# Optimization experiments

Measured on AMD Instinct MI355X. Metric: run time of the kernel, lower is better.

The kernel has to match this reference:

```python
import jax, jax.numpy as jnp
import numpy as np

N_SERIES = 1024  # N; x carries 3N stacked time-synchronous nodes
GCN_DEPTH = 2
IN_DIM = 64
H_DIM = 64


def setup_inputs() -> dict:
    key = jax.random.key(0)
    k = jax.random.split(key, 6)
    B, C, N3 = 64, IN_DIM, 3 * N_SERIES
    x = jax.random.normal(k[0], (N3, B, C), dtype=jnp.float32)
    A = jax.random.normal(k[1], (N3, N3), dtype=jnp.float32) * 0.02
    # Linear2d (1x1 conv) params per depth; act='glu' -> out = 2*h_dim
    s0 = 1.0 / np.sqrt(IN_DIM)
    s1 = 1.0 / np.sqrt(H_DIM)
    W0 = jax.random.uniform(k[2], (2 * H_DIM, IN_DIM), jnp.float32, -s0, s0)
    b0 = jax.random.uniform(k[3], (2 * H_DIM,), jnp.float32, -s0, s0)
    W1 = jax.random.uniform(k[4], (2 * H_DIM, H_DIM), jnp.float32, -s1, s1)
    b1 = jax.random.uniform(k[5], (2 * H_DIM,), jnp.float32, -s1, s1)
    return {"x": x, "A": A, "W0": W0, "b0": b0, "W1": W1, "b1": b1}


def reference(x, A, W0, b0, W1, b1):
    # x: (3N, B, C) -> (B, C, 3N)
    h = jnp.transpose(x, (1, 2, 0))
    convs = []
    for W, b in ((W0, b0), (W1, b1)):
        # GCN2d flow='tgt_to_src': h[b,c,v] = sum_w h[b,c,w] * A[v,w]  (L=1 squeezed)
        g = jnp.einsum('bcw,vw->bcv', h, A)
        # Linear2d 1x1 conv: channels C -> 2*h_dim, then GLU gate
        y = jnp.einsum('oc,bcv->bov', W, g) + b[None, :, None]
        lhs, rhs = jnp.split(y, 2, axis=1)
        h = lhs * jax.nn.sigmoid(rhs)          # (B, h_dim, 3N)
        convs.append(jnp.transpose(h, (2, 0, 1)))  # (3N, B, h_dim)
    # crop the middle N nodes of each depth, then max over depth
    cropped = jnp.stack([c[N_SERIES:2 * N_SERIES] for c in convs], axis=0)
    return jnp.max(cropped, axis=0)  # (N, B, h_dim)
```

## Files before the change

kernel.cpp:

```cpp
#include <hip/hip_runtime.h>
#include <hip/hip_bf16.h>
#include <stdint.h>

typedef __attribute__((ext_vector_type(8))) short s16x8;
typedef __attribute__((ext_vector_type(4))) float f32x4;
typedef __attribute__((ext_vector_type(8))) unsigned short u16x8;
typedef __attribute__((ext_vector_type(4))) unsigned short u16x4;

__device__ __forceinline__ float bf2f(unsigned short u) {
  union { uint32_t u; float f; } v; v.u = ((uint32_t)u) << 16; return v.f;
}
__device__ __forceinline__ unsigned short f2bf(float f) {
  union { float f; uint32_t u; } v; v.f = f;
  uint32_t u = v.u;
  return (unsigned short)((u + 0x7fffu + ((u >> 16) & 1u)) >> 16);
}
__device__ __forceinline__ void load_lds16(const void* g, void* l) {
  __builtin_amdgcn_global_load_lds(
      (const __attribute__((address_space(1))) void*)g,
      (__attribute__((address_space(3))) void*)l, 16, 0, 0);
}

template <int N>
__device__ __forceinline__ void vmw() {
  if constexpr (N == 0) asm volatile("s_waitcnt vmcnt(0)" ::: "memory");
  else if constexpr (N == 1) asm volatile("s_waitcnt vmcnt(1)" ::: "memory");
  else if constexpr (N == 2) asm volatile("s_waitcnt vmcnt(2)" ::: "memory");
  else if constexpr (N == 3) asm volatile("s_waitcnt vmcnt(3)" ::: "memory");
  else if constexpr (N == 4) asm volatile("s_waitcnt vmcnt(4)" ::: "memory");
  else if constexpr (N == 5) asm volatile("s_waitcnt vmcnt(5)" ::: "memory");
  else if constexpr (N == 6) asm volatile("s_waitcnt vmcnt(6)" ::: "memory");
  else if constexpr (N == 7) asm volatile("s_waitcnt vmcnt(7)" ::: "memory");
  else asm volatile("s_waitcnt vmcnt(8)" ::: "memory");
}
#define SBAR() asm volatile("s_barrier" ::: "memory")

__device__ __forceinline__ int sigma(int rt) {
  return rt < 16 ? rt : (rt < 32 ? rt + 16 : rt - 16);
}


__global__ __launch_bounds__(256) void k_prep(const void* __restrict__ xin,
                                              const void* __restrict__ Ain,
                                              const void* __restrict__ W0,
                                              const void* __restrict__ b0,
                                              const void* __restrict__ W1,
                                              const void* __restrict__ b1,
                                              unsigned short* __restrict__ xtp,
                                              unsigned short* __restrict__ Abp,
                                              unsigned short* __restrict__ wb) {
  __shared__ __align__(16) unsigned short sh[64 * 65];
  const int t = threadIdx.x;
  const int bid = blockIdx.x;
  int fp;
  {
    uint32_t u = ((const uint32_t*)xin)[(t & 63) * 97 + 1];
    int e = (u >> 7) & 0xFF;
    unsigned long long m = __ballot(e > 150);
    fp = (__popcll(m) > 6) ? 1 : 0;
  }

  if (bid < 3072) {
    const int w0 = (bid % 48) * 64;
    const int m0 = (bid / 48) * 64;
    if (fp) {
      const float* xf = (const float*)xin;
#pragma unroll
      for (int rep = 0; rep < 4; ++rep) {
        int vi = t + rep * 256;
        int r = vi >> 4;
        int c4 = (vi & 15) * 4;
        f32x4 v = *(const f32x4*)(xf + (uint64_t)(w0 + r) * 4096 + m0 + c4);
#pragma unroll
        for (int u = 0; u < 4; ++u) sh[(c4 + u) * 65 + r] = f2bf(v[u]);
      }
    } else {
      const unsigned short* xb = (const unsigned short*)xin;
#pragma unroll
      for (int rep = 0; rep < 2; ++rep) {
        int vi = t + rep * 256;
        int r = vi >> 3;
        int c8 = (vi & 7) * 8;
        u16x8 v = *(const u16x8*)(xb + (uint64_t)(w0 + r) * 4096 + m0 + c8);
#pragma unroll
        for (int u = 0; u < 8; ++u) sh[(c8 + u) * 65 + r] = v[u];
      }
    }
    __syncthreads();
    unsigned short* dst = xtp + ((uint64_t)(m0 >> 6) * 48 + (w0 >> 6)) * 4096;
#pragma unroll
    for (int rep = 0; rep < 2; ++rep) {
      int vi = t + rep * 256;
      int kb = vi >> 6, r = vi & 63;
      u16x8 v;
#pragma unroll
      for (int u = 0; u < 8; ++u) v[u] = sh[r * 65 + kb * 8 + u];
      *(u16x8*)(dst + kb * 512 + r * 8) = v;
    }
  } else if (bid < 5376) {
    const int b2 = bid - 3072;
    const int kt = b2 % 48, rt = b2 / 48;
    if (fp) {
      const float* Af = (const float*)Ain;
#pragma unroll
      for (int rep = 0; rep < 4; ++rep) {
        int vi = t + rep * 256;
        int r = vi >> 4;
        int c4 = (vi & 15) * 4;
        f32x4 v = *(const f32x4*)(Af + (uint64_t)(rt * 64 + r) * 3072 + kt * 64 + c4);
        int kb = c4 >> 3, e = c4 & 7;
#pragma unroll
        for (int u = 0; u < 4; ++u) sh[kb * 520 + r * 8 + e + u] = f2bf(v[u]);
      }
    } else {
      const unsigned short* Ab16 = (const unsigned short*)Ain;
#pragma unroll
      for (int rep = 0; rep < 2; ++rep) {
        int vi = t + rep * 256;
        int r = vi >> 3;
        int c8 = (vi & 7) * 8;
        u16x8 v = *(const u16x8*)(Ab16 + (uint64_t)(rt * 64 + r) * 3072 + kt * 64 + c8);
#pragma unroll
        for (int u = 0; u < 8; ++u) sh[(c8 >> 3) * 520 + r * 8 + u] = v[u];
      }
    }
    __syncthreads();
    unsigned short* dst = Abp + ((uint64_t)sigma(rt) * 48 + kt) * 4096;
#pragma unroll
    for (int rep = 0; rep < 2; ++rep) {
      int vi = t + rep * 256;
      int kb = vi >> 6, r = vi & 63;
      u16x8 v;
#pragma unroll
      for (int u = 0; u < 8; ++u) v[u] = sh[kb * 520 + r * 8 + u];
      *(u16x8*)(dst + kb * 512 + r * 8) = v;
    }
  } else {
    for (int i = t; i < 16640; i += 256) {
      const void* src; int off;
      if (i < 8192)        { src = W0; off = i; }
      else if (i < 8320)   { src = b0; off = i - 8192; }
      else if (i < 16512)  { src = W1; off = i - 8320; }
      else                 { src = b1; off = i - 16512; }
      wb[i] = fp ? f2bf(((const float*)src)[off]) : ((const unsigned short*)src)[off];
    }
  }
}

template <int BM, int MODE>
__global__ __launch_bounds__(512, 2) void k_gemm_glu6(
    const unsigned short* __restrict__ Am,
    const unsigned short* __restrict__ Bm,
    const unsigned short* __restrict__ W,
    const unsigned short* __restrict__ bias,
    unsigned short* __restrict__ H,
    float* __restrict__ Pout0,
    float* __restrict__ Pout1,
    int Vtot) {
  constexpr int KT64 = 48;
  constexpr int IF  = BM / 32;
  constexpr int NPH = (IF > 4) ? 2 : 1;
  constexpr int IPH = IF / NPH;
  constexpr int APL = (BM / 64) * 4;
  constexpr int P   = APL + 16;
  constexpr int QF  = P / 8;
  constexpr int QR  = P - QF * 8;
  constexpr int PPW = QF + (QR ? 1 : 0);
  constexpr int BUFS = P * 512;
  constexpr int NRB = BM / 16;
  constexpr int EPL = BM * 264;
  constexpr int SME = (MODE == 1) ? 4 * BUFS
                                  : ((4 * BUFS > EPL) ? 4 * BUFS : EPL);

  __shared__ __align__(16) unsigned short smem[SME];

  const int t    = threadIdx.x;
  const int lane = t & 63;
  const int wid  = t >> 6;
  const int wV   = wid >> 2;
  const int wM   = wid & 3;
  const int fr   = lane & 15;
  const int q4   = lane >> 4;
  const int m0   = blockIdx.y * 256;
  const int brt0 = m0 >> 6;

  int v0, kt0, ntk, artB;
  if constexpr (MODE == 1) {
    v0   = (blockIdx.x >> 1) * BM;
    kt0  = (blockIdx.x & 1) * 48;
    ntk  = 48;
    artB = 16;
  } else {
    v0 = blockIdx.x * BM; kt0 = 0; ntk = 96; artB = 0;
  }
  const int art0 = artB + (v0 >> 6);

  const int myq = QF + ((QR && wid < QR) ? 1 : 0);
  const unsigned short* srcb[PPW];
  int ldso[PPW];
#pragma unroll
  for (int q = 0; q < PPW; ++q) {
    int pi = wid + 8 * q;
    if (pi >= P) pi = P - 1;
    const int isA = pi < APL;
    const int rtl = (isA ? pi : pi - APL) >> 2;
    const int pb  = pi & 3;
    const unsigned short* base =
        isA ? (Am + (uint64_t)sigma(art0 + rtl) * KT64 * 4096)
            : (Bm + (uint64_t)(brt0 + rtl) * KT64 * 4096);
    srcb[q] = base + pb * 512 + lane * 8;
    ldso[q] = pi * 512;
  }

  int aoff[IF], boff[4];
#pragma unroll
  for (int i = 0; i < IF; ++i) {
    const int row = wV * (BM / 2) + i * 16 + fr;
    aoff[i] = ((row >> 6) * 4 + q4) * 512 + (row & 63) * 8;
  }
#pragma unroll
  for (int j = 0; j < 4; ++j)
    boff[j] = (APL + wM * 4 + q4) * 512 + (j * 16 + fr) * 8;

  f32x4 acc[IF][4] = {};

#pragma unroll
  for (int pt = 0; pt < 3; ++pt)
#pragma unroll
    for (int q = 0; q < PPW; ++q)
      if (q < myq)
        load_lds16(srcb[q] + (uint64_t)(kt0 + pt) * 2048, smem + pt * BUFS + ldso[q]);
  if (QR && wid < QR) { vmw<2 * (QF + 1)>(); } else { vmw<2 * QF>(); }
  SBAR();

#pragma unroll 4
  for (int tt = 0; tt < ntk; ++tt) {
    const unsigned short* buf = smem + (tt & 3) * BUFS;
    s16x8 bfr[4];
#pragma unroll
    for (int ph = 0; ph < NPH; ++ph) {
      if (ph == 0) {
#pragma unroll
        for (int j = 0; j < 4; ++j)
          bfr[j] = *(const s16x8*)(buf + boff[j]);
      }
      s16x8 afr[IPH];
#pragma unroll
      for (int ii = 0; ii < IPH; ++ii)
        afr[ii] = *(const s16x8*)(buf + aoff[ph * IPH + ii]);
      if (tt + 3 < ntk) {
        unsigned short* dst = smem + ((tt + 3) & 3) * BUFS;
#pragma unroll
        for (int q = 0; q < PPW; ++q)
          if ((q % NPH) == ph && q < myq)
            load_lds16(srcb[q] + (uint64_t)(kt0 + tt + 3) * 2048, dst + ldso[q]);
      }
      SBAR();
      __builtin_amdgcn_s_setprio(1);
#pragma unroll
      for (int ii = 0; ii < IPH; ++ii)
#pragma unroll
        for (int j = 0; j < 4; ++j)
          acc[ph * IPH + ii][j] = __builtin_amdgcn_mfma_f32_16x16x32_bf16(
              afr[ii], bfr[j], acc[ph * IPH + ii][j], 0, 0, 0);
      __builtin_amdgcn_s_setprio(0);
      if (ph == NPH - 1) {
        if (tt + 3 < ntk) {
          if (QR && wid < QR) { vmw<2 * (QF + 1)>(); } else { vmw<2 * QF>(); }
        } else if (tt + 2 < ntk) {
          if (QR && wid < QR) { vmw<QF + 1>(); } else { vmw<QF>(); }
        } else {
          vmw<0>();
        }
      }
      SBAR();
    }
  }

  if constexpr (MODE == 1) {
    float* Pout = (blockIdx.x & 1) ? Pout1 : Pout0;
#pragma unroll
    for (int i = 0; i < IF; ++i)
#pragma unroll
      for (int j = 0; j < 4; ++j) {
        const int col = wM * 64 + j * 16 + fr;
#pragma unroll
        for (int r = 0; r < 4; ++r) {
          const int row = wV * (BM / 2) + i * 16 + q4 * 4 + r;
          Pout[(uint64_t)(v0 + row) * 4096 + m0 + col] = acc[i][j][r];
        }
      }
    return;
  } else {
    __syncthreads();
    {
      const int rr = q4 * 4;
#pragma unroll
      for (int i = 0; i < IF; ++i)
#pragma unroll
        for (int j = 0; j < 4; ++j) {
          const int col = wM * 64 + j * 16 + fr;
#pragma unroll
          for (int r = 0; r < 4; ++r) {
            const int row = wV * (BM / 2) + i * 16 + rr + r;
            smem[row * 264 + col] = f2bf(acc[i][j][r]);
          }
        }
    }
    __syncthreads();

    s16x8 wf[2][8];
#pragma unroll
    for (int ksi = 0; ksi < 2; ++ksi)
#pragma unroll
      for (int j = 0; j < 8; ++j)
        wf[ksi][j] = *(const s16x8*)(W + (j * 16 + fr) * 64 + ksi * 32 + q4 * 8);
    float bj[8];
#pragma unroll
    for (int j = 0; j < 8; ++j) bj[j] = bf2f(bias[j * 16 + fr]);

    const int Vt = Vtot >> 6;
#pragma unroll
    for (int rep = 0; rep < (NRB + 7) / 8; ++rep) {
      const int rb = rep * 8 + wid;
      if (rb < NRB) {
#pragma unroll
        for (int bb = 0; bb < 4; ++bb) {
          f32x4 acc2[8] = {};
#pragma unroll
          for (int ksi = 0; ksi < 2; ++ksi) {
            s16x8 af = *(const s16x8*)(smem + (rb * 16 + fr) * 264 + bb * 64 +
                                       ksi * 32 + q4 * 8);
#pragma unroll
            for (int j = 0; j < 8; ++j)
              acc2[j] = __builtin_amdgcn_mfma_f32_16x16x32_bf16(af, wf[ksi][j],
                                                                acc2[j], 0, 0, 0);
          }
          const int v = v0 + rb * 16 + q4 * 4;
#pragma unroll
          for (int j = 0; j < 4; ++j) {
            u16x4 pk;
#pragma unroll
            for (int r = 0; r < 4; ++r) {
              float lhs = acc2[j][r] + bj[j];
              float rhs = acc2[j + 4][r] + bj[j + 4];
              float sg = 1.0f / (1.0f + __expf(-rhs));
              pk[r] = f2bf(lhs * sg);
            }
            const int o = j * 16 + fr;
            const int hrow = m0 + bb * 64 + o;
            *(u16x4*)(H + ((uint64_t)(hrow >> 6) * Vt + (v >> 6)) * 4096 +
                      ((v >> 3) & 7) * 512 + (hrow & 63) * 8 + (v & 7)) = pk;
          }
        }
      }
    }
  }
}

__global__ __launch_bounds__(512) void k_glufin(const float* __restrict__ P0f,
                                                const float* __restrict__ P1f,
                                                const unsigned short* __restrict__ W,
                                                const unsigned short* __restrict__ bias,
                                                const unsigned short* __restrict__ Hprev,
                                                float* __restrict__ outp) {
  __shared__ __align__(16) unsigned short g[64 * 264];
  const int t    = threadIdx.x;
  const int lane = t & 63;
  const int wid  = t >> 6;
  const int fr   = lane & 15;
  const int q4   = lane >> 4;
  const int v0   = blockIdx.x * 64;
  const int m0   = blockIdx.y * 256;

#pragma unroll
  for (int rep = 0; rep < 8; ++rep) {
    int vi = t + rep * 512;
    int row = vi >> 6;
    int c4 = (vi & 63) * 4;
    uint64_t idx = (uint64_t)(v0 + row) * 4096 + m0 + c4;
    f32x4 a = *(const f32x4*)(P0f + idx);
    f32x4 b = *(const f32x4*)(P1f + idx);
#pragma unroll
    for (int u = 0; u < 4; ++u) g[row * 264 + c4 + u] = f2bf(a[u] + b[u]);
  }
  __syncthreads();

  s16x8 wf[2][8];
#pragma unroll
  for (int ksi = 0; ksi < 2; ++ksi)
#pragma unroll
    for (int j = 0; j < 8; ++j)
      wf[ksi][j] = *(const s16x8*)(W + (j * 16 + fr) * 64 + ksi * 32 + q4 * 8);
  float bj[8];
#pragma unroll
  for (int j = 0; j < 8; ++j) bj[j] = bf2f(bias[j * 16 + fr]);

  const int rb = wid & 3;
#pragma unroll
  for (int bb2 = 0; bb2 < 2; ++bb2) {
    const int bb = (wid >> 2) * 2 + bb2;
    f32x4 acc2[8] = {};
#pragma unroll
    for (int ksi = 0; ksi < 2; ++ksi) {
      s16x8 af = *(const s16x8*)(g + (rb * 16 + fr) * 264 + bb * 64 +
                                 ksi * 32 + q4 * 8);
#pragma unroll
      for (int j = 0; j < 8; ++j)
        acc2[j] = __builtin_amdgcn_mfma_f32_16x16x32_bf16(af, wf[ksi][j],
                                                          acc2[j], 0, 0, 0);
    }
    const int v = v0 + rb * 16 + q4 * 4;
#pragma unroll
    for (int j = 0; j < 4; ++j) {
      const int o = j * 16 + fr;
      const int hrow = m0 + bb * 64 + o;
      const int c = 1024 + v;
      u16x4 hv = *(const u16x4*)(Hprev +
          ((uint64_t)(hrow >> 6) * 48 + (c >> 6)) * 4096 +
          ((c >> 3) & 7) * 512 + (hrow & 63) * 8 + (c & 7));
      float* op = outp + (uint64_t)v * 4096 + hrow;
#pragma unroll
      for (int r = 0; r < 4; ++r) {
        float lhs = acc2[j][r] + bj[j];
        float rhs = acc2[j + 4][r] + bj[j + 4];
        float sg = 1.0f / (1.0f + __expf(-rhs));
        op[(uint64_t)r * 4096] = fmaxf(lhs * sg, bf2f(hv[r]));
      }
    }
  }
}

extern "C" void kernel_launch(void* const* d_in, const int* in_sizes, int n_in,
                              void* d_out, int out_size, void* d_ws, size_t ws_size,
                              hipStream_t stream) {
  (void)in_sizes; (void)n_in; (void)out_size; (void)ws_size;
  const void* x  = d_in[0];
  const void* A  = d_in[1];
  const void* W0 = d_in[2];
  const void* b0 = d_in[3];
  const void* W1 = d_in[4];
  const void* b1 = d_in[5];
  float* out = (float*)d_out;

  char* ws = (char*)d_ws;
  unsigned short* Xtp = (unsigned short*)(ws + 0);
  unsigned short* Abp = (unsigned short*)(ws + 25165824);
  unsigned short* Wb  = (unsigned short*)(ws + 44040192);
  unsigned short* H1p = (unsigned short*)(ws + 44105728);
  float* Pk0 = (float*)(ws + 0);
  float* Pk1 = (float*)(ws + 16777216);

  k_prep<<<5377, 256, 0, stream>>>(x, A, W0, b0, W1, b1, Xtp, Abp, Wb);
  k_gemm_glu6<192, 0><<<dim3(16, 16), 512, 0, stream>>>(
      Abp, Xtp, Wb, Wb + 8192, H1p, nullptr, nullptr, 3072);
  k_gemm_glu6<128, 1><<<dim3(16, 16), 512, 0, stream>>>(
      Abp, H1p, nullptr, nullptr, nullptr, Pk0, Pk1, 1024);
  k_glufin<<<dim3(16, 16), 512, 0, stream>>>(Pk0, Pk1, Wb + 8320, Wb + 16512,
                                             H1p, out);
}
```

Measured before the change: 269.1 us.

## Fuse second-layer split-K GEMM with GLU epilogue, drop partial buffers

```diff
diff --git a/kernel.cpp b/kernel.cpp
--- a/kernel.cpp
+++ b/kernel.cpp
@@ -34,10 +34,6 @@
   else asm volatile("s_waitcnt vmcnt(8)" ::: "memory");
 }
 #define SBAR() asm volatile("s_barrier" ::: "memory")
-
-__device__ __forceinline__ int sigma(int rt) {
-  return rt < 16 ? rt : (rt < 32 ? rt + 16 : rt - 16);
-}
 
 
 __global__ __launch_bounds__(256) void k_prep(const void* __restrict__ xin,
@@ -125,7 +121,7 @@
       }
     }
     __syncthreads();
-    unsigned short* dst = Abp + ((uint64_t)sigma(rt) * 48 + kt) * 4096;
+    unsigned short* dst = Abp + ((uint64_t)rt * 48 + kt) * 4096;
 #pragma unroll
     for (int rep = 0; rep < 2; ++rep) {
       int vi = t + rep * 256;
@@ -147,30 +143,24 @@
   }
 }
 
-template <int BM, int MODE>
-__global__ __launch_bounds__(512, 2) void k_gemm_glu6(
+__global__ __launch_bounds__(512, 2) void k1_gemm_glu(
     const unsigned short* __restrict__ Am,
     const unsigned short* __restrict__ Bm,
     const unsigned short* __restrict__ W,
     const unsigned short* __restrict__ bias,
-    unsigned short* __restrict__ H,
-    float* __restrict__ Pout0,
-    float* __restrict__ Pout1,
-    int Vtot) {
-  constexpr int KT64 = 48;
-  constexpr int IF  = BM / 32;
-  constexpr int NPH = (IF > 4) ? 2 : 1;
-  constexpr int IPH = IF / NPH;
-  constexpr int APL = (BM / 64) * 4;
-  constexpr int P   = APL + 16;
-  constexpr int QF  = P / 8;
-  constexpr int QR  = P - QF * 8;
-  constexpr int PPW = QF + (QR ? 1 : 0);
+    unsigned short* __restrict__ H) {
+  constexpr int BM  = 192;
+  constexpr int IF  = 6;
+  constexpr int IPH = 3;
+  constexpr int APL = 12;
+  constexpr int P   = 28;
+  constexpr int QF  = 3;
+  constexpr int PPW = 4;
   constexpr int BUFS = P * 512;
-  constexpr int NRB = BM / 16;
-  constexpr int EPL = BM * 264;
-  constexpr int SME = (MODE == 1) ? 4 * BUFS
-                                  : ((4 * BUFS > EPL) ? 4 * BUFS : EPL);
+  constexpr int NT  = 96;
+  constexpr int Kt  = 48;
+  constexpr int NRB = 12;
+  constexpr int SME = 4 * BUFS;
 
   __shared__ __align__(16) unsigned short smem[SME];
 
@@ -181,21 +171,12 @@
   const int wM   = wid & 3;
   const int fr   = lane & 15;
   const int q4   = lane >> 4;
+  const int v0   = blockIdx.x * BM;
   const int m0   = blockIdx.y * 256;
+  const int art0 = v0 >> 6;
   const int brt0 = m0 >> 6;
 
-  int v0, kt0, ntk, artB;
-  if constexpr (MODE == 1) {
-    v0   = (blockIdx.x >> 1) * BM;
-    kt0  = (blockIdx.x & 1) * 48;
-    ntk  = 48;
-    artB = 16;
-  } else {
-    v0 = blockIdx.x * BM; kt0 = 0; ntk = 96; artB = 0;
-  }
-  const int art0 = artB + (v0 >> 6);
-
-  const int myq = QF + ((QR && wid < QR) ? 1 : 0);
+  const int myq = QF + ((wid < 4) ? 1 : 0);
   const unsigned short* srcb[PPW];
   int ldso[PPW];
 #pragma unroll
@@ -206,8 +187,8 @@
     const int rtl = (isA ? pi : pi - APL) >> 2;
     const int pb  = pi & 3;
     const unsigned short* base =
-        isA ? (Am + (uint64_t)sigma(art0 + rtl) * KT64 * 4096)
-            : (Bm + (uint64_t)(brt0 + rtl) * KT64 * 4096);
+        isA ? (Am + (uint64_t)(art0 + rtl) * Kt * 4096)
+            : (Bm + (uint64_t)(brt0 + rtl) * Kt * 4096);
     srcb[q] = base + pb * 512 + lane * 8;
     ldso[q] = pi * 512;
   }
@@ -215,7 +196,7 @@
   int aoff[IF], boff[4];
 #pragma unroll
   for (int i = 0; i < IF; ++i) {
-    const int row = wV * (BM / 2) + i * 16 + fr;
+    const int row = wV * 96 + i * 16 + fr;
     aoff[i] = ((row >> 6) * 4 + q4) * 512 + (row & 63) * 8;
   }
 #pragma unroll
@@ -229,16 +210,16 @@
 #pragma unroll
     for (int q = 0; q < PPW; ++q)
       if (q < myq)
-        load_lds16(srcb[q] + (uint64_t)(kt0 + pt) * 2048, smem + pt * BUFS + ldso[q]);
-  if (QR && wid < QR) { vmw<2 * (QF + 1)>(); } else { vmw<2 * QF>(); }
+        load_lds16(srcb[q] + pt * 2048, smem + pt * BUFS + ldso[q]);
+  if (wid < 4) { vmw<8>(); } else { vmw<6>(); }
   SBAR();
 
 #pragma unroll 4
-  for (int tt = 0; tt < ntk; ++tt) {
+  for (int tt = 0; tt < NT; ++tt) {
     const unsigned short* buf = smem + (tt & 3) * BUFS;
     s16x8 bfr[4];
 #pragma unroll
-    for (int ph = 0; ph < NPH; ++ph) {
+    for (int ph = 0; ph < 2; ++ph) {
       if (ph == 0) {
 #pragma unroll
         for (int j = 0; j < 4; ++j)
@@ -248,12 +229,12 @@
 #pragma unroll
       for (int ii = 0; ii < IPH; ++ii)
         afr[ii] = *(const s16x8*)(buf + aoff[ph * IPH + ii]);
-      if (tt + 3 < ntk) {
+      if (tt + 3 < NT) {
         unsigned short* dst = smem + ((tt + 3) & 3) * BUFS;
 #pragma unroll
         for (int q = 0; q < PPW; ++q)
-          if ((q % NPH) == ph && q < myq)
-            load_lds16(srcb[q] + (uint64_t)(kt0 + tt + 3) * 2048, dst + ldso[q]);
+          if ((q % 2) == ph && q < myq)
+            load_lds16(srcb[q] + (uint64_t)(tt + 3) * 2048, dst + ldso[q]);
       }
       SBAR();
       __builtin_amdgcn_s_setprio(1);
@@ -264,11 +245,11 @@
           acc[ph * IPH + ii][j] = __builtin_amdgcn_mfma_f32_16x16x32_bf16(
               afr[ii], bfr[j], acc[ph * IPH + ii][j], 0, 0, 0);
       __builtin_amdgcn_s_setprio(0);
-      if (ph == NPH - 1) {
-        if (tt + 3 < ntk) {
-          if (QR && wid < QR) { vmw<2 * (QF + 1)>(); } else { vmw<2 * QF>(); }
-        } else if (tt + 2 < ntk) {
-          if (QR && wid < QR) { vmw<QF + 1>(); } else { vmw<QF>(); }
+      if (ph == 1) {
+        if (tt + 3 < NT) {
+          if (wid < 4) { vmw<8>(); } else { vmw<6>(); }
+        } else if (tt + 2 < NT) {
+          if (wid < 4) { vmw<4>(); } else { vmw<3>(); }
         } else {
           vmw<0>();
         }
@@ -277,8 +258,9 @@
     }
   }
 
-  if constexpr (MODE == 1) {
-    float* Pout = (blockIdx.x & 1) ? Pout1 : Pout0;
+  __syncthreads();
+  {
+    const int rr = q4 * 4;
 #pragma unroll
     for (int i = 0; i < IF; ++i)
 #pragma unroll
@@ -286,103 +268,177 @@
         const int col = wM * 64 + j * 16 + fr;
 #pragma unroll
         for (int r = 0; r < 4; ++r) {
-          const int row = wV * (BM / 2) + i * 16 + q4 * 4 + r;
-          Pout[(uint64_t)(v0 + row) * 4096 + m0 + col] = acc[i][j][r];
+          const int row = wV * 96 + i * 16 + rr + r;
+          smem[row * 264 + col] = f2bf(acc[i][j][r]);
         }
       }
-    return;
-  } else {
-    __syncthreads();
-    {
-      const int rr = q4 * 4;
-#pragma unroll
-      for (int i = 0; i < IF; ++i)
+  }
+  __syncthreads();
+
+  s16x8 wf[2][8];
+#pragma unroll
+  for (int ksi = 0; ksi < 2; ++ksi)
+#pragma unroll
+    for (int j = 0; j < 8; ++j)
+      wf[ksi][j] = *(const s16x8*)(W + (j * 16 + fr) * 64 + ksi * 32 + q4 * 8);
+  float bj[8];
+#pragma unroll
+  for (int j = 0; j < 8; ++j) bj[j] = bf2f(bias[j * 16 + fr]);
+
+#pragma unroll
+  for (int rep = 0; rep < 2; ++rep) {
+    const int rb = rep * 8 + wid;
+    if (rb < NRB) {
+#pragma unroll
+      for (int bb = 0; bb < 4; ++bb) {
+        f32x4 acc2[8] = {};
+#pragma unroll
+        for (int ksi = 0; ksi < 2; ++ksi) {
+          s16x8 af = *(const s16x8*)(smem + (rb * 16 + fr) * 264 + bb * 64 +
+                                     ksi * 32 + q4 * 8);
+#pragma unroll
+          for (int j = 0; j < 8; ++j)
+            acc2[j] = __builtin_amdgcn_mfma_f32_16x16x32_bf16(af, wf[ksi][j],
+                                                              acc2[j], 0, 0, 0);
+        }
+        const int v = v0 + rb * 16 + q4 * 4;
 #pragma unroll
         for (int j = 0; j < 4; ++j) {
-          const int col = wM * 64 + j * 16 + fr;
+          u16x4 pk;
 #pragma unroll
           for (int r = 0; r < 4; ++r) {
-            const int row = wV * (BM / 2) + i * 16 + rr + r;
-            smem[row * 264 + col] = f2bf(acc[i][j][r]);
+            float lhs = acc2[j][r] + bj[j];
+            float rhs = acc2[j + 4][r] + bj[j + 4];
+            float sg = 1.0f / (1.0f + __expf(-rhs));
+            pk[r] = f2bf(lhs * sg);
           }
+          const int o = j * 16 + fr;
+          const int hrow = m0 + bb * 64 + o;
+          *(u16x4*)(H + ((uint64_t)(hrow >> 6) * 48 + (v >> 6)) * 4096 +
+                    ((v >> 3) & 7) * 512 + (hrow & 63) * 8 + (v & 7)) = pk;
         }
-    }
-    __syncthreads();
-
-    s16x8 wf[2][8];
-#pragma unroll
-    for (int ksi = 0; ksi < 2; ++ksi)
-#pragma unroll
-      for (int j = 0; j < 8; ++j)
-        wf[ksi][j] = *(const s16x8*)(W + (j * 16 + fr) * 64 + ksi * 32 + q4 * 8);
-    float bj[8];
-#pragma unroll
-    for (int j = 0; j < 8; ++j) bj[j] = bf2f(bias[j * 16 + fr]);
-
-    const int Vt = Vtot >> 6;
-#pragma unroll
-    for (int rep = 0; rep < (NRB + 7) / 8; ++rep) {
-      const int rb = rep * 8 + wid;
-      if (rb < NRB) {
-#pragma unroll
-        for (int bb = 0; bb < 4; ++bb) {
-          f32x4 acc2[8] = {};
-#pragma unroll
-          for (int ksi = 0; ksi < 2; ++ksi) {
-            s16x8 af = *(const s16x8*)(smem + (rb * 16 + fr) * 264 + bb * 64 +
-                                       ksi * 32 + q4 * 8);
-#pragma unroll
-            for (int j = 0; j < 8; ++j)
-              acc2[j] = __builtin_amdgcn_mfma_f32_16x16x32_bf16(af, wf[ksi][j],
-                                                                acc2[j], 0, 0, 0);
-          }
-          const int v = v0 + rb * 16 + q4 * 4;
-#pragma unroll
-          for (int j = 0; j < 4; ++j) {
-            u16x4 pk;
-#pragma unroll
-            for (int r = 0; r < 4; ++r) {
-              float lhs = acc2[j][r] + bj[j];
-              float rhs = acc2[j + 4][r] + bj[j + 4];
-              float sg = 1.0f / (1.0f + __expf(-rhs));
-              pk[r] = f2bf(lhs * sg);
-            }
-            const int o = j * 16 + fr;
-            const int hrow = m0 + bb * 64 + o;
-            *(u16x4*)(H + ((uint64_t)(hrow >> 6) * Vt + (v >> 6)) * 4096 +
-                      ((v >> 3) & 7) * 512 + (hrow & 63) * 8 + (v & 7)) = pk;
-          }
-        }
-      }
-    }
-  }
-}
-
-__global__ __launch_bounds__(512) void k_glufin(const float* __restrict__ P0f,
-                                                const float* __restrict__ P1f,
-                                                const unsigned short* __restrict__ W,
-                                                const unsigned short* __restrict__ bias,
-                                                const unsigned short* __restrict__ Hprev,
-                                                float* __restrict__ outp) {
-  __shared__ __align__(16) unsigned short g[64 * 264];
+      }
+    }
+  }
+}
+
+__global__ __launch_bounds__(512, 2) void k3_gemm_glu(
+    const unsigned short* __restrict__ Am,
+    const unsigned short* __restrict__ Bm,
+    const unsigned short* __restrict__ W,
+    const unsigned short* __restrict__ bias,
+    const unsigned short* __restrict__ Hprev,
+    float* __restrict__ outp) {
+  constexpr int BM  = 64;
+  constexpr int IF  = 2;
+  constexpr int APL = 4;
+  constexpr int P   = 20;
+  constexpr int QF  = 2;
+  constexpr int PPW = 3;
+  constexpr int BUFS = P * 512;
+  constexpr int NT  = 96;
+  constexpr int Kt  = 48;
+  constexpr int SME = 4 * BUFS;
+
+  __shared__ __align__(16) unsigned short smem[SME];
+
   const int t    = threadIdx.x;
   const int lane = t & 63;
   const int wid  = t >> 6;
+  const int wV   = wid >> 2;
+  const int wM   = wid & 3;
   const int fr   = lane & 15;
   const int q4   = lane >> 4;
-  const int v0   = blockIdx.x * 64;
+  const int v0   = blockIdx.x * BM;
   const int m0   = blockIdx.y * 256;
-
-#pragma unroll
-  for (int rep = 0; rep < 8; ++rep) {
-    int vi = t + rep * 512;
-    int row = vi >> 6;
-    int c4 = (vi & 63) * 4;
-    uint64_t idx = (uint64_t)(v0 + row) * 4096 + m0 + c4;
-    f32x4 a = *(const f32x4*)(P0f + idx);
-    f32x4 b = *(const f32x4*)(P1f + idx);
-#pragma unroll
-    for (int u = 0; u < 4; ++u) g[row * 264 + c4 + u] = f2bf(a[u] + b[u]);
+  const int art0 = 16 + (v0 >> 6);
+  const int brt0 = m0 >> 6;
+
+  const int myq = QF + ((wid < 4) ? 1 : 0);
+  const unsigned short* srcb[PPW];
+  int ldso[PPW];
+#pragma unroll
+  for (int q = 0; q < PPW; ++q) {
+    int pi = wid + 8 * q;
+    if (pi >= P) pi = P - 1;
+    const int isA = pi < APL;
+    const int rtl = (isA ? pi : pi - APL) >> 2;
+    const int pb  = pi & 3;
+    const unsigned short* base =
+        isA ? (Am + (uint64_t)(art0 + rtl) * Kt * 4096)
+            : (Bm + (uint64_t)(brt0 + rtl) * Kt * 4096);
+    srcb[q] = base + pb * 512 + lane * 8;
+    ldso[q] = pi * 512;
+  }
+
+  int aoff[IF], boff[4];
+#pragma unroll
+  for (int i = 0; i < IF; ++i) {
+    const int row = wV * 32 + i * 16 + fr;
+    aoff[i] = ((row >> 6) * 4 + q4) * 512 + (row & 63) * 8;
+  }
+#pragma unroll
+  for (int j = 0; j < 4; ++j)
+    boff[j] = (APL + wM * 4 + q4) * 512 + (j * 16 + fr) * 8;
+
+  f32x4 acc[IF][4] = {};
+
+#pragma unroll
+  for (int pt = 0; pt < 3; ++pt)
+#pragma unroll
+    for (int q = 0; q < PPW; ++q)
+      if (q < myq)
+        load_lds16(srcb[q] + pt * 2048, smem + pt * BUFS + ldso[q]);
+  if (wid < 4) { vmw<6>(); } else { vmw<4>(); }
+  SBAR();
+
+#pragma unroll 4
+  for (int tt = 0; tt < NT; ++tt) {
+    const unsigned short* buf = smem + (tt & 3) * BUFS;
+    s16x8 bfr[4], afr[IF];
+#pragma unroll
+    for (int j = 0; j < 4; ++j) bfr[j] = *(const s16x8*)(buf + boff[j]);
+#pragma unroll
+    for (int i = 0; i < IF; ++i) afr[i] = *(const s16x8*)(buf + aoff[i]);
+    if (tt + 3 < NT) {
+      unsigned short* pdst = smem + ((tt + 3) & 3) * BUFS;
+#pragma unroll
+      for (int q = 0; q < PPW; ++q)
+        if (q < myq)
+          load_lds16(srcb[q] + (uint64_t)(tt + 3) * 2048, pdst + ldso[q]);
+    }
+    __builtin_amdgcn_s_setprio(1);
+#pragma unroll
+    for (int i = 0; i < IF; ++i)
+#pragma unroll
+      for (int j = 0; j < 4; ++j)
+        acc[i][j] = __builtin_amdgcn_mfma_f32_16x16x32_bf16(afr[i], bfr[j],
+                                                            acc[i][j], 0, 0, 0);
+    __builtin_amdgcn_s_setprio(0);
+    if (tt + 3 < NT) {
+      if (wid < 4) { vmw<6>(); } else { vmw<4>(); }
+    } else if (tt + 2 < NT) {
+      if (wid < 4) { vmw<3>(); } else { vmw<2>(); }
+    } else {
+      vmw<0>();
+    }
+    SBAR();
+  }
+
+  __syncthreads();
+  {
+    const int rr = q4 * 4;
+#pragma unroll
+    for (int i = 0; i < IF; ++i)
+#pragma unroll
+      for (int j = 0; j < 4; ++j) {
+        const int col = wM * 64 + j * 16 + fr;
+#pragma unroll
+        for (int r = 0; r < 4; ++r) {
+          const int row = wV * 32 + i * 16 + rr + r;
+          smem[row * 264 + col] = f2bf(acc[i][j][r]);
+        }
+      }
   }
   __syncthreads();
 
@@ -396,36 +452,39 @@
 #pragma unroll
   for (int j = 0; j < 8; ++j) bj[j] = bf2f(bias[j * 16 + fr]);
 
-  const int rb = wid & 3;
-#pragma unroll
-  for (int bb2 = 0; bb2 < 2; ++bb2) {
-    const int bb = (wid >> 2) * 2 + bb2;
-    f32x4 acc2[8] = {};
-#pragma unroll
-    for (int ksi = 0; ksi < 2; ++ksi) {
-      s16x8 af = *(const s16x8*)(g + (rb * 16 + fr) * 264 + bb * 64 +
-                                 ksi * 32 + q4 * 8);
-#pragma unroll
-      for (int j = 0; j < 8; ++j)
-        acc2[j] = __builtin_amdgcn_mfma_f32_16x16x32_bf16(af, wf[ksi][j],
-                                                          acc2[j], 0, 0, 0);
-    }
-    const int v = v0 + rb * 16 + q4 * 4;
-#pragma unroll
-    for (int j = 0; j < 4; ++j) {
-      const int o = j * 16 + fr;
-      const int hrow = m0 + bb * 64 + o;
-      const int c = 1024 + v;
-      u16x4 hv = *(const u16x4*)(Hprev +
-          ((uint64_t)(hrow >> 6) * 48 + (c >> 6)) * 4096 +
-          ((c >> 3) & 7) * 512 + (hrow & 63) * 8 + (c & 7));
-      float* op = outp + (uint64_t)v * 4096 + hrow;
-#pragma unroll
-      for (int r = 0; r < 4; ++r) {
-        float lhs = acc2[j][r] + bj[j];
-        float rhs = acc2[j + 4][r] + bj[j + 4];
-        float sg = 1.0f / (1.0f + __expf(-rhs));
-        op[(uint64_t)r * 4096] = fmaxf(lhs * sg, bf2f(hv[r]));
+  {
+    const int rb = wid & 3;
+    const int bbh = wid >> 2;
+#pragma unroll
+    for (int bb2 = 0; bb2 < 2; ++bb2) {
+      const int bb = bbh * 2 + bb2;
+      f32x4 acc2[8] = {};
+#pragma unroll
+      for (int ksi = 0; ksi < 2; ++ksi) {
+        s16x8 af = *(const s16x8*)(smem + (rb * 16 + fr) * 264 + bb * 64 +
+                                   ksi * 32 + q4 * 8);
+#pragma unroll
+        for (int j = 0; j < 8; ++j)
+          acc2[j] = __builtin_amdgcn_mfma_f32_16x16x32_bf16(af, wf[ksi][j],
+                                                            acc2[j], 0, 0, 0);
+      }
+      const int v = v0 + rb * 16 + q4 * 4;
+#pragma unroll
+      for (int j = 0; j < 4; ++j) {
+        const int o = j * 16 + fr;
+        const int hrow = m0 + bb * 64 + o;
+        const int c = 1024 + v;
+        u16x4 hv = *(const u16x4*)(Hprev +
+            ((uint64_t)(hrow >> 6) * 48 + (c >> 6)) * 4096 +
+            ((c >> 3) & 7) * 512 + (hrow & 63) * 8 + (c & 7));
+        float* op = outp + (uint64_t)v * 4096 + hrow;
+#pragma unroll
+        for (int r = 0; r < 4; ++r) {
+          float lhs = acc2[j][r] + bj[j];
+          float rhs = acc2[j + 4][r] + bj[j + 4];
+          float sg = 1.0f / (1.0f + __expf(-rhs));
+          op[(uint64_t)r * 4096] = fmaxf(lhs * sg, bf2f(hv[r]));
+        }
       }
     }
   }
@@ -448,14 +507,9 @@
   unsigned short* Abp = (unsigned short*)(ws + 25165824);
   unsigned short* Wb  = (unsigned short*)(ws + 44040192);
   unsigned short* H1p = (unsigned short*)(ws + 44105728);
-  float* Pk0 = (float*)(ws + 0);
-  float* Pk1 = (float*)(ws + 16777216);
 
   k_prep<<<5377, 256, 0, stream>>>(x, A, W0, b0, W1, b1, Xtp, Abp, Wb);
-  k_gemm_glu6<192, 0><<<dim3(16, 16), 512, 0, stream>>>(
-      Abp, Xtp, Wb, Wb + 8192, H1p, nullptr, nullptr, 3072);
-  k_gemm_glu6<128, 1><<<dim3(16, 16), 512, 0, stream>>>(
-      Abp, H1p, nullptr, nullptr, nullptr, Pk0, Pk1, 1024);
-  k_glufin<<<dim3(16, 16), 512, 0, stream>>>(Pk0, Pk1, Wb + 8320, Wb + 16512,
-                                             H1p, out);
-}
+  k1_gemm_glu<<<dim3(16, 16), 512, 0, stream>>>(Abp, Xtp, Wb, Wb + 8192, H1p);
+  k3_gemm_glu<<<dim3(16, 16), 512, 0, stream>>>(
+      Abp, H1p, Wb + 8320, Wb + 16512, H1p, out);
+}
```

Measured after the change: 265.8 us. Within noise of the previous version (-1.2%).
